# Performance work log

Hardware: AMD Instinct MI355X
Metric: run time of the kernel (lower is better)

## Reference

```python
import jax, jax.numpy as jnp
import numpy as np

BS, C, H, W = 2, 128, 80, 160
P, G = 9, 8
GC = C // G
EPS = 1e-5


def _layernorm_c(x, g, b):
    # x: (bs, C, H, W); LayerNorm over channel dim (to_3d dim=2 -> norm over c)
    m = jnp.mean(x, axis=1, keepdims=True)
    v = jnp.mean((x - m) ** 2, axis=1, keepdims=True)
    return (x - m) / jnp.sqrt(v + EPS) * g[None, :, None, None] + b[None, :, None, None]


def _conv1x1(x, w, b):
    return jnp.einsum('bchw,oc->bohw', x, w) + b[None, :, None, None]


def _bilinear_sample(feat, pts):
    # feat (bs,C,H,W); pts (bs,N,2) normalized [0,1]; zero padding outside (DAF convention)
    bs, c, h, w = feat.shape
    x = pts[..., 0] * w - 0.5
    y = pts[..., 1] * h - 0.5
    x0 = jnp.floor(x)
    y0 = jnp.floor(y)
    dx = x - x0
    dy = y - y0
    x0i = x0.astype(jnp.int32)
    y0i = y0.astype(jnp.int32)

    def corner(xi, yi, wgt):
        valid = (xi >= 0) & (xi < w) & (yi >= 0) & (yi < h)
        xc = jnp.clip(xi, 0, w - 1)
        yc = jnp.clip(yi, 0, h - 1)
        g = jax.vmap(lambda f, yy, xx: f[:, yy, xx].T)(feat, yc, xc)  # (bs,N,C)
        return g * (wgt * valid)[..., None]

    return (corner(x0i, y0i, (1 - dx) * (1 - dy))
            + corner(x0i + 1, y0i, dx * (1 - dy))
            + corner(x0i, y0i + 1, (1 - dx) * dy)
            + corner(x0i + 1, y0i + 1, dx * dy))


def _branch(match_flat, anchor, feat_value, wmap, kp_w, kp_b):
    bs = feat_value.shape[0]
    hw = H * W
    # Sparse1DKeyPointsGenerator: learned 1D offsets along the disparity (x) direction
    off = match_flat @ kp_w.T + kp_b  # (bs, HW, P)
    anc = anchor.reshape(bs, hw, P, 2)
    kp = jnp.stack([anc[..., 0] + off, anc[..., 1]], axis=-1)  # (bs,HW,P,2)
    # group-softmax attention weights over num_pts
    wts = wmap.transpose(0, 2, 3, 1).reshape(bs, hw, P, G)  # channel c = p*G + g
    wts = jax.nn.softmax(wts, axis=2)
    # deformable aggregation: bilinear gather at key points + group-weighted sum over pts
    sampled = _bilinear_sample(feat_value, kp.reshape(bs, hw * P, 2))
    sampled = sampled.reshape(bs, hw, P, G, GC)
    out = jnp.einsum('bnpgc,bnpg->bngc', sampled, wts).reshape(bs, hw, C)
    out = out.reshape(bs, H, W, C).transpose(0, 3, 1, 2)
    return out, kp


def _forward(mask, match, context, geometric, context_anchor_points, geometric_anchor_points,
             ln_g, ln_b, lnc_g, lnc_b, lng_g, lng_b,
             wc_w, wc_b, wg_w, wg_b, vc_w, vc_b, vg_w, vg_b,
             out_w, out_b, kpc_w, kpc_b, kpg_w, kpg_b):
    bs = match.shape[0]
    hw = H * W
    match_n = _layernorm_c(match, ln_g, ln_b)
    context_n = _layernorm_c(context, lnc_g, lnc_b)
    geometric_n = _layernorm_c(geometric, lng_g, lng_b)
    ctx_val = _conv1x1(context_n, vc_w, vc_b)
    geo_val = _conv1x1(geometric_n, vg_w, vg_b)
    match_flat = match_n.reshape(bs, C, hw).transpose(0, 2, 1)  # (bs,HW,C)
    wc = _conv1x1(match_n, wc_w, wc_b)  # (bs,G*P,H,W)
    wg = _conv1x1(match_n, wg_w, wg_b)
    ctx_out, ctx_kp = _branch(match_flat, context_anchor_points, ctx_val, wc, kpc_w, kpc_b)
    geo_out, geo_kp = _branch(match_flat, geometric_anchor_points, geo_val, wg, kpg_w, kpg_b)
    out = jnp.concatenate([ctx_out * mask, geo_out], axis=1)
    out = _conv1x1(out, out_w, out_b)  # proj_drop is identity (p=0)
    return out, ctx_kp.reshape(bs, H, W, P, 2), geo_kp.reshape(bs, H, W, P, 2)


def setup_inputs() -> dict:
    key = jax.random.key(0)
    ks = jax.random.split(key, 20)

    def wn(k, shape):
        return jax.random.normal(k, shape, jnp.float32) * 0.02

    return {
        'mask': jax.random.uniform(ks[0], (BS, 1, H, W), jnp.float32),
        'match': jax.random.normal(ks[1], (BS, C, H, W), jnp.float32),
        'context': jax.random.normal(ks[2], (BS, C, H, W), jnp.float32),
        'geometric': jax.random.normal(ks[3], (BS, C, H, W), jnp.float32),
        'context_anchor_points': jax.random.uniform(ks[4], (BS, H, W, P, 2), jnp.float32),
        'geometric_anchor_points': jax.random.uniform(ks[5], (BS, H, W, P, 2), jnp.float32),
        'ln_g': jnp.ones((C,), jnp.float32), 'ln_b': jnp.zeros((C,), jnp.float32),
        'lnc_g': jnp.ones((C,), jnp.float32), 'lnc_b': jnp.zeros((C,), jnp.float32),
        'lng_g': jnp.ones((C,), jnp.float32), 'lng_b': jnp.zeros((C,), jnp.float32),
        'wc_w': wn(ks[6], (G * P, C)), 'wc_b': jnp.zeros((G * P,), jnp.float32),
        'wg_w': wn(ks[7], (G * P, C)), 'wg_b': jnp.zeros((G * P,), jnp.float32),
        'vc_w': wn(ks[8], (C, C)), 'vc_b': jnp.zeros((C,), jnp.float32),
        'vg_w': wn(ks[9], (C, C)), 'vg_b': jnp.zeros((C,), jnp.float32),
        'out_w': wn(ks[10], (C, 2 * C)), 'out_b': jnp.zeros((C,), jnp.float32),
        'kpc_w': wn(ks[11], (P, C)), 'kpc_b': jnp.zeros((P,), jnp.float32),
        'kpg_w': wn(ks[12], (P, C)), 'kpg_b': jnp.zeros((P,), jnp.float32),
    }


def reference(mask, match, context, geometric, context_anchor_points, geometric_anchor_points,
              ln_g, ln_b, lnc_g, lnc_b, lng_g, lng_b,
              wc_w, wc_b, wg_w, wg_b, vc_w, vc_b, vg_w, vg_b,
              out_w, out_b, kpc_w, kpc_b, kpg_w, kpg_b):
    return _forward(mask, match, context, geometric, context_anchor_points, geometric_anchor_points,
                    ln_g, ln_b, lnc_g, lnc_b, lng_g, lng_b,
                    wc_w, wc_b, wg_w, wg_b, vc_w, vc_b, vg_w, vg_b,
                    out_w, out_b, kpc_w, kpc_b, kpg_w, kpg_b)
```

## Files before the change

kernel.cpp:

```cpp
#include <hip/hip_runtime.h>
#include <hip/hip_bf16.h>

typedef __hip_bfloat16 bf16;
typedef __bf16 b16x8 __attribute__((ext_vector_type(8)));
typedef __bf16 b16x4 __attribute__((ext_vector_type(4)));
typedef float f32x4 __attribute__((ext_vector_type(4)));
typedef float f32x2 __attribute__((ext_vector_type(2)));

#define HWs   12800
#define NPIX  25600
#define IMG_H 80
#define IMG_W 160

#define OFF_VCB  0
#define OFF_VGB  16384
#define OFF_MATB 32768
#define OFF_OUTB 53504
#define NW_BF16  86272

__global__ __launch_bounds__(256) void k_prep(
    const float* __restrict__ vc_w, const float* __restrict__ vg_w,
    const float* __restrict__ wc_w, const float* __restrict__ wg_w,
    const float* __restrict__ kpc_w, const float* __restrict__ kpg_w,
    const float* __restrict__ out_w,
    const float* __restrict__ wc_b, const float* __restrict__ wg_b,
    const float* __restrict__ kpc_b, const float* __restrict__ kpg_b,
    bf16* __restrict__ wbuf, float* __restrict__ bias176)
{
    int i = blockIdx.x * 256 + threadIdx.x;
    if (i < 16384) {
        wbuf[i] = __float2bfloat16(vc_w[i]);
    } else if (i < 32768) {
        wbuf[i] = __float2bfloat16(vg_w[i - 16384]);
    } else if (i < 53504) {
        int j = i - 32768; int row = j >> 7; int c = j & 127;
        float v;
        if (row < 72)       v = wc_w[row * 128 + c];
        else if (row < 144) v = wg_w[(row - 72) * 128 + c];
        else if (row < 153) v = kpc_w[(row - 144) * 128 + c];
        else                v = kpg_w[(row - 153) * 128 + c];
        wbuf[i] = __float2bfloat16(v);
    } else if (i < NW_BF16) {
        wbuf[i] = __float2bfloat16(out_w[i - 53504]);
    } else if (i < NW_BF16 + 176) {
        int j = i - NW_BF16;
        float v = 0.f;
        if (j < 72)       v = wc_b[j];
        else if (j < 144) v = wg_b[j - 72];
        else if (j < 153) v = kpc_b[j - 144];
        else if (j < 162) v = kpg_b[j - 153];
        bias176[j] = v;
    }
}

__global__ __launch_bounds__(256) void k_stage1(
    const float* __restrict__ match, const float* __restrict__ context, const float* __restrict__ geometric,
    const float* __restrict__ ln_g, const float* __restrict__ ln_b,
    const float* __restrict__ lnc_g, const float* __restrict__ lnc_b,
    const float* __restrict__ lng_g, const float* __restrict__ lng_b,
    const float* __restrict__ vc_b, const float* __restrict__ vg_b,
    const bf16* __restrict__ wbuf, const float* __restrict__ bias176,
    const float* __restrict__ anc_c, const float* __restrict__ anc_g,
    unsigned char* __restrict__ ctx8, unsigned char* __restrict__ geo8,
    bf16* __restrict__ wts_g, float* __restrict__ coords_g,
    float* __restrict__ kp_out)
{
    __shared__ __align__(16) bf16 tile_s[32 * 136];
    __shared__ __align__(16) bf16 logit_s[32 * 148];
    __shared__ float offs_s[32 * 18];
    __shared__ float red1[8][32];
    __shared__ float red2[8][32];

    int bx = blockIdx.x;
    int seg = bx % 3;
    int tile = bx / 3;
    int t = threadIdx.x;
    int pixbase = tile * 32;

    const float* X  = (seg == 0) ? context : (seg == 1) ? geometric : match;
    const float* gg = (seg == 0) ? lnc_g   : (seg == 1) ? lng_g     : ln_g;
    const float* bb = (seg == 0) ? lnc_b   : (seg == 1) ? lng_b     : ln_b;

    int p = t & 31;
    int cq = t >> 5;
    int b = pixbase >= HWs;
    int hw = pixbase - b * HWs;
    const float* base = X + ((size_t)b * 128) * HWs + hw + p;
    float xv[16];
#pragma unroll
    for (int j = 0; j < 16; j++) xv[j] = base[(size_t)(cq * 16 + j) * HWs];

    int wv = t >> 6;
    int lane = t & 63;
    int s = wv >> 1;
    int h = wv & 1;
    int lrow = lane & 15;
    int lq = lane >> 4;
    const bf16* Wb = (seg == 0) ? wbuf + OFF_VCB
                   : (seg == 1) ? wbuf + OFF_VGB
                                : wbuf + OFF_MATB;
    b16x8 wf[4][4];
#pragma unroll
    for (int i = 0; i < 4; i++) {
        int o = (h + 2 * i) * 16 + lrow;
        const bf16* wr = Wb + (size_t)o * 128;
#pragma unroll
        for (int kk = 0; kk < 4; kk++)
            wf[i][kk] = *(const b16x8*)(wr + (kk * 4 + lq) * 8);
    }

    {
        float s1 = 0.f, s2 = 0.f;
#pragma unroll
        for (int j = 0; j < 16; j++) { s1 += xv[j]; s2 += xv[j] * xv[j]; }
        red1[cq][p] = s1; red2[cq][p] = s2;
        __syncthreads();
        float S1 = 0.f, S2 = 0.f;
#pragma unroll
        for (int q = 0; q < 8; q++) { S1 += red1[q][p]; S2 += red2[q][p]; }
        float mean = S1 * (1.f / 128.f);
        float var  = fmaxf(S2 * (1.f / 128.f) - mean * mean, 0.f);
        float rstd = rsqrtf(var + 1e-5f);
#pragma unroll
        for (int j = 0; j < 16; j++) {
            int c = cq * 16 + j;
            float y = (xv[j] - mean) * rstd * gg[c] + bb[c];
            tile_s[p * 136 + c] = __float2bfloat16(y);
        }
        __syncthreads();
    }

    const b16x8* arow = (const b16x8*)(tile_s + (s * 16 + lrow) * 136);
    b16x8 af[4];
#pragma unroll
    for (int kk = 0; kk < 4; kk++) af[kk] = arow[kk * 4 + lq];

    int prow = s * 16 + lrow;

    if (seg < 2) {
        unsigned char* val = (seg == 0) ? ctx8 : geo8;
        const float* vb = (seg == 0) ? vc_b : vg_b;
        size_t prix = (size_t)(pixbase + prow) * 128;
#pragma unroll
        for (int i = 0; i < 4; i++) {
            int obase = (h + 2 * i) * 16 + lq * 4;
            f32x4 acc = {0.f, 0.f, 0.f, 0.f};
#pragma unroll
            for (int kk = 0; kk < 4; kk++)
                acc = __builtin_amdgcn_mfma_f32_16x16x32_bf16(wf[i][kk], af[kk], acc, 0, 0, 0);
            f32x4 bv = *(const f32x4*)(vb + obase);
            int u = __builtin_amdgcn_cvt_pk_fp8_f32(acc[0] + bv[0], acc[1] + bv[1], 0, false);
            u = __builtin_amdgcn_cvt_pk_fp8_f32(acc[2] + bv[2], acc[3] + bv[3], u, true);
            *(unsigned int*)(val + prix + obase) = (unsigned int)u;
        }
        return;
    }

#pragma unroll
    for (int i = 0; i < 4; i++) {
        int obase = (h + 2 * i) * 16 + lq * 4;
        f32x4 acc = {0.f, 0.f, 0.f, 0.f};
#pragma unroll
        for (int kk = 0; kk < 4; kk++)
            acc = __builtin_amdgcn_mfma_f32_16x16x32_bf16(wf[i][kk], af[kk], acc, 0, 0, 0);
        f32x4 bv = *(const f32x4*)(bias176 + obase);
        b16x4 pk4;
#pragma unroll
        for (int r = 0; r < 4; r++) pk4[r] = (__bf16)(acc[r] + bv[r]);
        *(b16x4*)(logit_s + prow * 148 + obase) = pk4;
    }
    for (int ot = h + 8; ot < 11; ot += 2) {
        int obase = ot * 16 + lq * 4;
        const bf16* wr = Wb + (size_t)(ot * 16 + lrow) * 128;
        f32x4 acc = {0.f, 0.f, 0.f, 0.f};
#pragma unroll
        for (int kk = 0; kk < 4; kk++)
            acc = __builtin_amdgcn_mfma_f32_16x16x32_bf16(*(const b16x8*)(wr + (kk * 4 + lq) * 8), af[kk], acc, 0, 0, 0);
        f32x4 bv = *(const f32x4*)(bias176 + obase);
        if (ot == 8) {
            b16x4 pk4;
#pragma unroll
            for (int r = 0; r < 4; r++) pk4[r] = (__bf16)(acc[r] + bv[r]);
            *(b16x4*)(logit_s + prow * 148 + obase) = pk4;
        } else if (ot == 9) {
#pragma unroll
            for (int r = 0; r < 4; r++)
                offs_s[prow * 18 + (obase - 144) + r] = acc[r] + bv[r];
        } else {
            if (lq == 0) {
                offs_s[prow * 18 + 16] = acc[0] + bv[0];
                offs_s[prow * 18 + 17] = acc[1] + bv[1];
            }
        }
    }
    __syncthreads();

#pragma unroll
    for (int i = 0; i < 2; i++) {
        int task = t + 256 * i;
        int lp = task >> 4;
        int sub = task & 15;
        int br = sub >> 3;
        int g = sub & 7;
        const bf16* basel = logit_s + lp * 148 + br * 72 + g;
        float v[9];
        float m = -1e30f;
#pragma unroll
        for (int pp = 0; pp < 9; pp++) { v[pp] = __bfloat162float(basel[pp * 8]); m = fmaxf(m, v[pp]); }
        float ssum = 0.f;
#pragma unroll
        for (int pp = 0; pp < 9; pp++) { v[pp] = __expf(v[pp] - m); ssum += v[pp]; }
        float inv = 1.f / ssum;
        int pix = pixbase + lp;
        bf16* wbp = wts_g + ((size_t)pix * 2 + br) * 72 + g * 9;
#pragma unroll
        for (int pp = 0; pp < 9; pp++) wbp[pp] = __float2bfloat16(v[pp] * inv);
    }

    for (int i = 0; i < 3; i++) {
        int task = t + 256 * i;
        if (task < 576) {
            int lp = task / 18;
            int sub2 = task - lp * 18;
            int br = sub2 / 9;
            int pp = sub2 - br * 9;
            int pix = pixbase + lp;
            float off = offs_s[lp * 18 + br * 9 + pp];
            const float* anc = br ? anc_g : anc_c;
            f32x2 a2 = *(const f32x2*)(anc + (size_t)pix * 18 + pp * 2);
            float kx = a2[0] + off;
            f32x2 kp2 = {kx, a2[1]};
            *(f32x2*)(kp_out + (size_t)br * (NPIX * 18) + (size_t)pix * 18 + pp * 2) = kp2;
            f32x2 c2 = {kx * 160.f - 0.5f, a2[1] * 80.f - 0.5f};
            *(f32x2*)(coords_g + ((size_t)pix * 2 + br) * 18 + pp * 2) = c2;
        }
    }
}

__global__ __launch_bounds__(256) void k_fuse(
    const unsigned char* __restrict__ ctx8, const unsigned char* __restrict__ geo8,
    const bf16* __restrict__ wts_g, const float* __restrict__ coords_g,
    const float* __restrict__ mask,
    const bf16* __restrict__ outb, const float* __restrict__ out_b,
    float* __restrict__ out)
{
    __shared__ __align__(16) bf16 agg_s[16 * 264];

    int t = threadIdx.x;
    int wv = t >> 6;
    int lane = t & 63;
    int q = lane >> 4;
    int sub = lane & 15;
    int c0 = sub * 8;
    int g = sub >> 1;

    int pixbase = blockIdx.x * 16;
    int qw = wv * 4 + q;
    int pix = pixbase + qw;
    int b = pixbase >= HWs;
    int rowbase = b * HWs;

#pragma unroll
    for (int br = 0; br < 2; br++) {
        const unsigned char* val = br ? geo8 : ctx8;
        int tk = pix * 2 + br;
        const float* cb = coords_g + (size_t)tk * 18;
        const bf16* wb = wts_g + (size_t)tk * 72 + g * 9;

        float wtv[9];
#pragma unroll
        for (int pp = 0; pp < 9; pp++) wtv[pp] = __bfloat162float(wb[pp]);

        float acc[8] = {0.f, 0.f, 0.f, 0.f, 0.f, 0.f, 0.f, 0.f};
        for (int pp = 0; pp < 9; pp++) {
            f32x2 cc = *(const f32x2*)(cb + pp * 2);
            float fx = floorf(cc[0]), fy = floorf(cc[1]);
            float dx = cc[0] - fx, dy = cc[1] - fy;
            int x0 = (int)fx, y0 = (int)fy;
            float wt = wtv[pp];
#pragma unroll
            for (int c4 = 0; c4 < 4; c4++) {
                int xi = x0 + (c4 & 1);
                int yi = y0 + (c4 >> 1);
                bool ok = (xi >= 0) & (xi < IMG_W) & (yi >= 0) & (yi < IMG_H);
                int xc = min(max(xi, 0), IMG_W - 1);
                int yc = min(max(yi, 0), IMG_H - 1);
                float wx = (c4 & 1) ? dx : 1.f - dx;
                float wy = (c4 >> 1) ? dy : 1.f - dy;
                float wgt = ok ? wx * wy * wt : 0.f;
                uint2 u = *(const uint2*)(val + (size_t)(rowbase + yc * IMG_W + xc) * 128 + c0);
                f32x2 v01 = __builtin_amdgcn_cvt_pk_f32_fp8(u.x, false);
                f32x2 v23 = __builtin_amdgcn_cvt_pk_f32_fp8(u.x, true);
                f32x2 v45 = __builtin_amdgcn_cvt_pk_f32_fp8(u.y, false);
                f32x2 v67 = __builtin_amdgcn_cvt_pk_f32_fp8(u.y, true);
                acc[0] += wgt * v01[0]; acc[1] += wgt * v01[1];
                acc[2] += wgt * v23[0]; acc[3] += wgt * v23[1];
                acc[4] += wgt * v45[0]; acc[5] += wgt * v45[1];
                acc[6] += wgt * v67[0]; acc[7] += wgt * v67[1];
            }
        }
        float mv = (br == 0) ? mask[pix] : 1.f;
        b16x8 pk;
#pragma unroll
        for (int j = 0; j < 8; j++) pk[j] = (__bf16)(acc[j] * mv);
        *(b16x8*)(agg_s + qw * 264 + br * 128 + c0) = pk;
    }
    __syncthreads();

    int lrow = lane & 15;
    int lq = lane >> 4;
    b16x8 af[8];
#pragma unroll
    for (int kk = 0; kk < 8; kk++)
        af[kk] = *(const b16x8*)(agg_s + lrow * 264 + (kk * 4 + lq) * 8);
#pragma unroll
    for (int i = 0; i < 2; i++) {
        int o = (wv + 4 * i) * 16 + lrow;
        const bf16* wrow = outb + (size_t)o * 256;
        f32x4 acc = {0.f, 0.f, 0.f, 0.f};
#pragma unroll
        for (int kk = 0; kk < 8; kk++)
            acc = __builtin_amdgcn_mfma_f32_16x16x32_bf16(af[kk], *(const b16x8*)(wrow + (kk * 4 + lq) * 8), acc, 0, 0, 0);
        float bias = out_b[o];
        f32x4 st;
#pragma unroll
        for (int r = 0; r < 4; r++) st[r] = acc[r] + bias;
        int hw0 = pixbase + lq * 4 - rowbase;
        *(f32x4*)(out + (size_t)b * (128 * HWs) + (size_t)o * HWs + hw0) = st;
    }
}

extern "C" void kernel_launch(void* const* d_in, const int* in_sizes, int n_in,
                              void* d_out, int out_size, void* d_ws, size_t ws_size,
                              hipStream_t stream)
{
    const float* mask      = (const float*)d_in[0];
    const float* match     = (const float*)d_in[1];
    const float* context   = (const float*)d_in[2];
    const float* geometric = (const float*)d_in[3];
    const float* anc_c     = (const float*)d_in[4];
    const float* anc_g     = (const float*)d_in[5];
    const float* ln_g  = (const float*)d_in[6];
    const float* ln_b  = (const float*)d_in[7];
    const float* lnc_g = (const float*)d_in[8];
    const float* lnc_b = (const float*)d_in[9];
    const float* lng_g = (const float*)d_in[10];
    const float* lng_b = (const float*)d_in[11];
    const float* wc_w  = (const float*)d_in[12];
    const float* wc_b  = (const float*)d_in[13];
    const float* wg_w  = (const float*)d_in[14];
    const float* wg_b  = (const float*)d_in[15];
    const float* vc_w  = (const float*)d_in[16];
    const float* vc_b  = (const float*)d_in[17];
    const float* vg_w  = (const float*)d_in[18];
    const float* vg_b  = (const float*)d_in[19];
    const float* out_w = (const float*)d_in[20];
    const float* out_b = (const float*)d_in[21];
    const float* kpc_w = (const float*)d_in[22];
    const float* kpc_b = (const float*)d_in[23];
    const float* kpg_w = (const float*)d_in[24];
    const float* kpg_b = (const float*)d_in[25];

    char* w = (char*)d_ws;
    unsigned char* ctx8 = (unsigned char*)(w);
    unsigned char* geo8 = (unsigned char*)(w + 3276800);
    bf16*  wts_g    = (bf16*)(w + 6553600);
    float* coords_g = (float*)(w + 13926400);
    bf16*  wbuf     = (bf16*)(w + 30720000);
    float* bias176  = (float*)(w + 30892544);

    float* outp = (float*)d_out;
    float* kp_out = outp + (size_t)2 * 128 * HWs;

    k_prep<<<(NW_BF16 + 176 + 255) / 256, 256, 0, stream>>>(
        vc_w, vg_w, wc_w, wg_w, kpc_w, kpg_w, out_w,
        wc_b, wg_b, kpc_b, kpg_b, wbuf, bias176);
    k_stage1<<<2400, 256, 0, stream>>>(match, context, geometric,
                                       ln_g, ln_b, lnc_g, lnc_b, lng_g, lng_b,
                                       vc_b, vg_b, wbuf, bias176,
                                       anc_c, anc_g,
                                       ctx8, geo8, wts_g, coords_g, kp_out);
    k_fuse<<<1600, 256, 0, stream>>>(ctx8, geo8, wts_g, coords_g, mask,
                                     wbuf + OFF_OUTB, out_b, outp);
}
```

Baseline: 199.1 us.

## Drop weight prep kernel, coalesce stage1 stores, widen fuse gathers

Removes the separate weight-conversion kernel and converts fp32 weights to bf16 on the fly inside both kernels. The fp8 value tiles and softmax weights are staged through swizzled shared memory so the global stores are coalesced 16-byte writes, and LN reduction buffers alias the logit buffer. The coordinates buffer is removed, so k_fuse recomputes sample coordinates from kp_out. k_fuse is also reorganised so each thread handles one branch and 16 channels with 16-byte gathers instead of looping over both branches with 8-byte loads. In exchange, weights are reloaded as fp32 and converted repeatedly in every block, and there are extra barriers.

Result: slower. 228.6 us (+14.8%).

```diff
diff --git a/kernel.cpp b/kernel.cpp
--- a/kernel.cpp
+++ b/kernel.cpp
@@ -3,7 +3,6 @@
 
 typedef __hip_bfloat16 bf16;
 typedef __bf16 b16x8 __attribute__((ext_vector_type(8)));
-typedef __bf16 b16x4 __attribute__((ext_vector_type(4)));
 typedef float f32x4 __attribute__((ext_vector_type(4)));
 typedef float f32x2 __attribute__((ext_vector_type(2)));
 
@@ -12,45 +11,25 @@
 #define IMG_H 80
 #define IMG_W 160
 
-#define OFF_VCB  0
-#define OFF_VGB  16384
-#define OFF_MATB 32768
-#define OFF_OUTB 53504
-#define NW_BF16  86272
-
-__global__ __launch_bounds__(256) void k_prep(
-    const float* __restrict__ vc_w, const float* __restrict__ vg_w,
-    const float* __restrict__ wc_w, const float* __restrict__ wg_w,
-    const float* __restrict__ kpc_w, const float* __restrict__ kpg_w,
-    const float* __restrict__ out_w,
-    const float* __restrict__ wc_b, const float* __restrict__ wg_b,
-    const float* __restrict__ kpc_b, const float* __restrict__ kpg_b,
-    bf16* __restrict__ wbuf, float* __restrict__ bias176)
+static __device__ inline b16x8 ldw8(const float* __restrict__ p)
 {
-    int i = blockIdx.x * 256 + threadIdx.x;
-    if (i < 16384) {
-        wbuf[i] = __float2bfloat16(vc_w[i]);
-    } else if (i < 32768) {
-        wbuf[i] = __float2bfloat16(vg_w[i - 16384]);
-    } else if (i < 53504) {
-        int j = i - 32768; int row = j >> 7; int c = j & 127;
-        float v;
-        if (row < 72)       v = wc_w[row * 128 + c];
-        else if (row < 144) v = wg_w[(row - 72) * 128 + c];
-        else if (row < 153) v = kpc_w[(row - 144) * 128 + c];
-        else                v = kpg_w[(row - 153) * 128 + c];
-        wbuf[i] = __float2bfloat16(v);
-    } else if (i < NW_BF16) {
-        wbuf[i] = __float2bfloat16(out_w[i - 53504]);
-    } else if (i < NW_BF16 + 176) {
-        int j = i - NW_BF16;
-        float v = 0.f;
-        if (j < 72)       v = wc_b[j];
-        else if (j < 144) v = wg_b[j - 72];
-        else if (j < 153) v = kpc_b[j - 144];
-        else if (j < 162) v = kpg_b[j - 153];
-        bias176[j] = v;
-    }
+    f32x4 a = *(const f32x4*)p;
+    f32x4 c = *(const f32x4*)(p + 4);
+    b16x8 r;
+    r[0] = (__bf16)a[0]; r[1] = (__bf16)a[1]; r[2] = (__bf16)a[2]; r[3] = (__bf16)a[3];
+    r[4] = (__bf16)c[0]; r[5] = (__bf16)c[1]; r[6] = (__bf16)c[2]; r[7] = (__bf16)c[3];
+    return r;
+}
+
+static __device__ inline const float* mat_row(
+    const float* __restrict__ wc, const float* __restrict__ wg,
+    const float* __restrict__ kpc, const float* __restrict__ kpg, int o)
+{
+    o = min(o, 161);
+    if (o < 72)  return wc  + (size_t)o * 128;
+    if (o < 144) return wg  + (size_t)(o - 72) * 128;
+    if (o < 153) return kpc + (size_t)(o - 144) * 128;
+    return kpg + (size_t)(o - 153) * 128;
 }
 
 __global__ __launch_bounds__(256) void k_stage1(
@@ -58,18 +37,25 @@
     const float* __restrict__ ln_g, const float* __restrict__ ln_b,
     const float* __restrict__ lnc_g, const float* __restrict__ lnc_b,
     const float* __restrict__ lng_g, const float* __restrict__ lng_b,
+    const float* __restrict__ vc_w, const float* __restrict__ vg_w,
     const float* __restrict__ vc_b, const float* __restrict__ vg_b,
-    const bf16* __restrict__ wbuf, const float* __restrict__ bias176,
+    const float* __restrict__ wc_w, const float* __restrict__ wg_w,
+    const float* __restrict__ kpc_w, const float* __restrict__ kpg_w,
+    const float* __restrict__ wc_b, const float* __restrict__ wg_b,
+    const float* __restrict__ kpc_b, const float* __restrict__ kpg_b,
     const float* __restrict__ anc_c, const float* __restrict__ anc_g,
     unsigned char* __restrict__ ctx8, unsigned char* __restrict__ geo8,
-    bf16* __restrict__ wts_g, float* __restrict__ coords_g,
-    float* __restrict__ kp_out)
+    bf16* __restrict__ wts_g, float* __restrict__ kp_out)
 {
     __shared__ __align__(16) bf16 tile_s[32 * 136];
-    __shared__ __align__(16) bf16 logit_s[32 * 148];
+    __shared__ __align__(16) char u_s[32 * 152 * 2];
     __shared__ float offs_s[32 * 18];
-    __shared__ float red1[8][32];
-    __shared__ float red2[8][32];
+    __shared__ float bias_s[176];
+
+    bf16* logit_s = (bf16*)u_s;
+    float (*red1)[32] = (float(*)[32])u_s;
+    float (*red2)[32] = (float(*)[32])(u_s + 1024);
+    unsigned char* fp8_s = (unsigned char*)u_s;
 
     int bx = blockIdx.x;
     int seg = bx % 3;
@@ -96,17 +82,26 @@
     int h = wv & 1;
     int lrow = lane & 15;
     int lq = lane >> 4;
-    const bf16* Wb = (seg == 0) ? wbuf + OFF_VCB
-                   : (seg == 1) ? wbuf + OFF_VGB
-                                : wbuf + OFF_MATB;
     b16x8 wf[4][4];
 #pragma unroll
     for (int i = 0; i < 4; i++) {
         int o = (h + 2 * i) * 16 + lrow;
-        const bf16* wr = Wb + (size_t)o * 128;
+        const float* wr = (seg == 0) ? vc_w + (size_t)o * 128
+                        : (seg == 1) ? vg_w + (size_t)o * 128
+                        : (o < 72)   ? wc_w + (size_t)o * 128
+                                     : wg_w + (size_t)(o - 72) * 128;
 #pragma unroll
         for (int kk = 0; kk < 4; kk++)
-            wf[i][kk] = *(const b16x8*)(wr + (kk * 4 + lq) * 8);
+            wf[i][kk] = ldw8(wr + (kk * 4 + lq) * 8);
+    }
+
+    if (seg == 2 && t < 176) {
+        float v = 0.f;
+        if (t < 72)       v = wc_b[t];
+        else if (t < 144) v = wg_b[t - 72];
+        else if (t < 153) v = kpc_b[t - 144];
+        else if (t < 162) v = kpg_b[t - 153];
+        bias_s[t] = v;
     }
 
     {
@@ -140,7 +135,7 @@
     if (seg < 2) {
         unsigned char* val = (seg == 0) ? ctx8 : geo8;
         const float* vb = (seg == 0) ? vc_b : vg_b;
-        size_t prix = (size_t)(pixbase + prow) * 128;
+        int swz = (prow & 7) << 4;
 #pragma unroll
         for (int i = 0; i < 4; i++) {
             int obase = (h + 2 * i) * 16 + lq * 4;
@@ -151,8 +146,13 @@
             f32x4 bv = *(const f32x4*)(vb + obase);
             int u = __builtin_amdgcn_cvt_pk_fp8_f32(acc[0] + bv[0], acc[1] + bv[1], 0, false);
             u = __builtin_amdgcn_cvt_pk_fp8_f32(acc[2] + bv[2], acc[3] + bv[3], u, true);
-            *(unsigned int*)(val + prix + obase) = (unsigned int)u;
-        }
+            *(unsigned int*)(fp8_s + prow * 128 + (obase ^ swz)) = (unsigned int)u;
+        }
+        __syncthreads();
+        int row = t >> 3;
+        int col = t & 7;
+        uint4 v4 = *(const uint4*)(fp8_s + row * 128 + ((col ^ (row & 7)) * 16));
+        *(uint4*)(val + (size_t)(pixbase + row) * 128 + col * 16) = v4;
         return;
     }
 
@@ -163,25 +163,23 @@
 #pragma unroll
         for (int kk = 0; kk < 4; kk++)
             acc = __builtin_amdgcn_mfma_f32_16x16x32_bf16(wf[i][kk], af[kk], acc, 0, 0, 0);
-        f32x4 bv = *(const f32x4*)(bias176 + obase);
-        b16x4 pk4;
-#pragma unroll
-        for (int r = 0; r < 4; r++) pk4[r] = (__bf16)(acc[r] + bv[r]);
-        *(b16x4*)(logit_s + prow * 148 + obase) = pk4;
+        f32x4 bv = *(const f32x4*)(bias_s + obase);
+#pragma unroll
+        for (int r = 0; r < 4; r++)
+            logit_s[prow * 152 + obase + r] = __float2bfloat16(acc[r] + bv[r]);
     }
     for (int ot = h + 8; ot < 11; ot += 2) {
         int obase = ot * 16 + lq * 4;
-        const bf16* wr = Wb + (size_t)(ot * 16 + lrow) * 128;
+        const float* wr = mat_row(wc_w, wg_w, kpc_w, kpg_w, ot * 16 + lrow);
         f32x4 acc = {0.f, 0.f, 0.f, 0.f};
 #pragma unroll
         for (int kk = 0; kk < 4; kk++)
-            acc = __builtin_amdgcn_mfma_f32_16x16x32_bf16(*(const b16x8*)(wr + (kk * 4 + lq) * 8), af[kk], acc, 0, 0, 0);
-        f32x4 bv = *(const f32x4*)(bias176 + obase);
+            acc = __builtin_amdgcn_mfma_f32_16x16x32_bf16(ldw8(wr + (kk * 4 + lq) * 8), af[kk], acc, 0, 0, 0);
+        f32x4 bv = *(const f32x4*)(bias_s + obase);
         if (ot == 8) {
-            b16x4 pk4;
-#pragma unroll
-            for (int r = 0; r < 4; r++) pk4[r] = (__bf16)(acc[r] + bv[r]);
-            *(b16x4*)(logit_s + prow * 148 + obase) = pk4;
+#pragma unroll
+            for (int r = 0; r < 4; r++)
+                logit_s[prow * 152 + obase + r] = __float2bfloat16(acc[r] + bv[r]);
         } else if (ot == 9) {
 #pragma unroll
             for (int r = 0; r < 4; r++)
@@ -195,6 +193,7 @@
     }
     __syncthreads();
 
+    float sm[2][9];
 #pragma unroll
     for (int i = 0; i < 2; i++) {
         int task = t + 256 * i;
@@ -202,7 +201,7 @@
         int sub = task & 15;
         int br = sub >> 3;
         int g = sub & 7;
-        const bf16* basel = logit_s + lp * 148 + br * 72 + g;
+        const bf16* basel = logit_s + lp * 152 + br * 72 + g;
         float v[9];
         float m = -1e30f;
 #pragma unroll
@@ -211,10 +210,31 @@
 #pragma unroll
         for (int pp = 0; pp < 9; pp++) { v[pp] = __expf(v[pp] - m); ssum += v[pp]; }
         float inv = 1.f / ssum;
-        int pix = pixbase + lp;
-        bf16* wbp = wts_g + ((size_t)pix * 2 + br) * 72 + g * 9;
-#pragma unroll
-        for (int pp = 0; pp < 9; pp++) wbp[pp] = __float2bfloat16(v[pp] * inv);
+#pragma unroll
+        for (int pp = 0; pp < 9; pp++) sm[i][pp] = v[pp] * inv;
+    }
+    __syncthreads();
+#pragma unroll
+    for (int i = 0; i < 2; i++) {
+        int task = t + 256 * i;
+        int lp = task >> 4;
+        int sub = task & 15;
+        int br = sub >> 3;
+        int g = sub & 7;
+        bf16* dst = logit_s + lp * 152 + br * 72 + g * 9;
+#pragma unroll
+        for (int pp = 0; pp < 9; pp++) dst[pp] = __float2bfloat16(sm[i][pp]);
+    }
+    __syncthreads();
+#pragma unroll
+    for (int i = 0; i < 3; i++) {
+        int idx = t + 256 * i;
+        if (idx < 576) {
+            int lp = idx / 18;
+            int c8 = idx - lp * 18;
+            *(b16x8*)(wts_g + (size_t)pixbase * 144 + (size_t)idx * 8) =
+                *(const b16x8*)(logit_s + lp * 152 + c8 * 8);
+        }
     }
 
     for (int i = 0; i < 3; i++) {
@@ -228,20 +248,17 @@
             float off = offs_s[lp * 18 + br * 9 + pp];
             const float* anc = br ? anc_g : anc_c;
             f32x2 a2 = *(const f32x2*)(anc + (size_t)pix * 18 + pp * 2);
-            float kx = a2[0] + off;
-            f32x2 kp2 = {kx, a2[1]};
+            f32x2 kp2 = {a2[0] + off, a2[1]};
             *(f32x2*)(kp_out + (size_t)br * (NPIX * 18) + (size_t)pix * 18 + pp * 2) = kp2;
-            f32x2 c2 = {kx * 160.f - 0.5f, a2[1] * 80.f - 0.5f};
-            *(f32x2*)(coords_g + ((size_t)pix * 2 + br) * 18 + pp * 2) = c2;
         }
     }
 }
 
 __global__ __launch_bounds__(256) void k_fuse(
     const unsigned char* __restrict__ ctx8, const unsigned char* __restrict__ geo8,
-    const bf16* __restrict__ wts_g, const float* __restrict__ coords_g,
+    const bf16* __restrict__ wts_g, const float* __restrict__ kp_out,
     const float* __restrict__ mask,
-    const bf16* __restrict__ outb, const float* __restrict__ out_b,
+    const float* __restrict__ out_w, const float* __restrict__ out_b,
     float* __restrict__ out)
 {
     __shared__ __align__(16) bf16 agg_s[16 * 264];
@@ -249,62 +266,70 @@
     int t = threadIdx.x;
     int wv = t >> 6;
     int lane = t & 63;
-    int q = lane >> 4;
-    int sub = lane & 15;
-    int c0 = sub * 8;
-    int g = sub >> 1;
+    int task = wv * 8 + (lane >> 3);
+    int br = task >> 4;
+    int pixidx = task & 15;
+    int g = lane & 7;
+    int c0 = g * 16;
 
     int pixbase = blockIdx.x * 16;
-    int qw = wv * 4 + q;
-    int pix = pixbase + qw;
+    int pix = pixbase + pixidx;
     int b = pixbase >= HWs;
     int rowbase = b * HWs;
 
-#pragma unroll
-    for (int br = 0; br < 2; br++) {
-        const unsigned char* val = br ? geo8 : ctx8;
-        int tk = pix * 2 + br;
-        const float* cb = coords_g + (size_t)tk * 18;
-        const bf16* wb = wts_g + (size_t)tk * 72 + g * 9;
-
-        float wtv[9];
-#pragma unroll
-        for (int pp = 0; pp < 9; pp++) wtv[pp] = __bfloat162float(wb[pp]);
-
-        float acc[8] = {0.f, 0.f, 0.f, 0.f, 0.f, 0.f, 0.f, 0.f};
-        for (int pp = 0; pp < 9; pp++) {
-            f32x2 cc = *(const f32x2*)(cb + pp * 2);
-            float fx = floorf(cc[0]), fy = floorf(cc[1]);
-            float dx = cc[0] - fx, dy = cc[1] - fy;
-            int x0 = (int)fx, y0 = (int)fy;
-            float wt = wtv[pp];
-#pragma unroll
-            for (int c4 = 0; c4 < 4; c4++) {
-                int xi = x0 + (c4 & 1);
-                int yi = y0 + (c4 >> 1);
-                bool ok = (xi >= 0) & (xi < IMG_W) & (yi >= 0) & (yi < IMG_H);
-                int xc = min(max(xi, 0), IMG_W - 1);
-                int yc = min(max(yi, 0), IMG_H - 1);
-                float wx = (c4 & 1) ? dx : 1.f - dx;
-                float wy = (c4 >> 1) ? dy : 1.f - dy;
-                float wgt = ok ? wx * wy * wt : 0.f;
-                uint2 u = *(const uint2*)(val + (size_t)(rowbase + yc * IMG_W + xc) * 128 + c0);
-                f32x2 v01 = __builtin_amdgcn_cvt_pk_f32_fp8(u.x, false);
-                f32x2 v23 = __builtin_amdgcn_cvt_pk_f32_fp8(u.x, true);
-                f32x2 v45 = __builtin_amdgcn_cvt_pk_f32_fp8(u.y, false);
-                f32x2 v67 = __builtin_amdgcn_cvt_pk_f32_fp8(u.y, true);
-                acc[0] += wgt * v01[0]; acc[1] += wgt * v01[1];
-                acc[2] += wgt * v23[0]; acc[3] += wgt * v23[1];
-                acc[4] += wgt * v45[0]; acc[5] += wgt * v45[1];
-                acc[6] += wgt * v67[0]; acc[7] += wgt * v67[1];
+    const unsigned char* val = br ? geo8 : ctx8;
+    const bf16* wb = wts_g + (size_t)(pix * 2 + br) * 72 + g * 9;
+    const float* cb = kp_out + (size_t)br * (NPIX * 18) + (size_t)pix * 18;
+
+    float wtv[9];
+#pragma unroll
+    for (int pp = 0; pp < 9; pp++) wtv[pp] = __bfloat162float(wb[pp]);
+
+    float acc[16];
+#pragma unroll
+    for (int j = 0; j < 16; j++) acc[j] = 0.f;
+
+#pragma unroll
+    for (int pp = 0; pp < 9; pp++) {
+        f32x2 kp2 = *(const f32x2*)(cb + pp * 2);
+        float px = kp2[0] * 160.f - 0.5f;
+        float py = kp2[1] * 80.f - 0.5f;
+        float fx = floorf(px), fy = floorf(py);
+        float dx = px - fx, dy = py - fy;
+        int x0 = (int)fx, y0 = (int)fy;
+        float wt = wtv[pp];
+#pragma unroll
+        for (int c4 = 0; c4 < 4; c4++) {
+            int xi = x0 + (c4 & 1);
+            int yi = y0 + (c4 >> 1);
+            bool ok = (xi >= 0) & (xi < IMG_W) & (yi >= 0) & (yi < IMG_H);
+            int xc = min(max(xi, 0), IMG_W - 1);
+            int yc = min(max(yi, 0), IMG_H - 1);
+            float wx = (c4 & 1) ? dx : 1.f - dx;
+            float wy = (c4 >> 1) ? dy : 1.f - dy;
+            float wgt = ok ? wx * wy * wt : 0.f;
+            uint4 u = *(const uint4*)(val + (size_t)(rowbase + yc * IMG_W + xc) * 128 + c0);
+            unsigned int uw[4] = {u.x, u.y, u.z, u.w};
+#pragma unroll
+            for (int w2 = 0; w2 < 4; w2++) {
+                f32x2 lo = __builtin_amdgcn_cvt_pk_f32_fp8(uw[w2], false);
+                f32x2 hi = __builtin_amdgcn_cvt_pk_f32_fp8(uw[w2], true);
+                acc[w2 * 4 + 0] += wgt * lo[0];
+                acc[w2 * 4 + 1] += wgt * lo[1];
+                acc[w2 * 4 + 2] += wgt * hi[0];
+                acc[w2 * 4 + 3] += wgt * hi[1];
             }
         }
-        float mv = (br == 0) ? mask[pix] : 1.f;
-        b16x8 pk;
-#pragma unroll
-        for (int j = 0; j < 8; j++) pk[j] = (__bf16)(acc[j] * mv);
-        *(b16x8*)(agg_s + qw * 264 + br * 128 + c0) = pk;
-    }
+    }
+    float mv = br ? 1.f : mask[pix];
+    b16x8 pk0, pk1;
+#pragma unroll
+    for (int j = 0; j < 8; j++) {
+        pk0[j] = (__bf16)(acc[j] * mv);
+        pk1[j] = (__bf16)(acc[8 + j] * mv);
+    }
+    *(b16x8*)(agg_s + pixidx * 264 + br * 128 + c0) = pk0;
+    *(b16x8*)(agg_s + pixidx * 264 + br * 128 + c0 + 8) = pk1;
     __syncthreads();
 
     int lrow = lane & 15;
@@ -316,15 +341,15 @@
 #pragma unroll
     for (int i = 0; i < 2; i++) {
         int o = (wv + 4 * i) * 16 + lrow;
-        const bf16* wrow = outb + (size_t)o * 256;
-        f32x4 acc = {0.f, 0.f, 0.f, 0.f};
+        const float* wrow = out_w + (size_t)o * 256;
+        f32x4 acc4 = {0.f, 0.f, 0.f, 0.f};
 #pragma unroll
         for (int kk = 0; kk < 8; kk++)
-            acc = __builtin_amdgcn_mfma_f32_16x16x32_bf16(af[kk], *(const b16x8*)(wrow + (kk * 4 + lq) * 8), acc, 0, 0, 0);
+            acc4 = __builtin_amdgcn_mfma_f32_16x16x32_bf16(af[kk], ldw8(wrow + (kk * 4 + lq) * 8), acc4, 0, 0, 0);
         float bias = out_b[o];
         f32x4 st;
 #pragma unroll
-        for (int r = 0; r < 4; r++) st[r] = acc[r] + bias;
+        for (int r = 0; r < 4; r++) st[r] = acc4[r] + bias;
         int hw0 = pixbase + lq * 4 - rowbase;
         *(f32x4*)(out + (size_t)b * (128 * HWs) + (size_t)o * HWs + hw0) = st;
     }
@@ -365,21 +390,17 @@
     unsigned char* ctx8 = (unsigned char*)(w);
     unsigned char* geo8 = (unsigned char*)(w + 3276800);
     bf16*  wts_g    = (bf16*)(w + 6553600);
-    float* coords_g = (float*)(w + 13926400);
-    bf16*  wbuf     = (bf16*)(w + 30720000);
-    float* bias176  = (float*)(w + 30892544);
 
     float* outp = (float*)d_out;
     float* kp_out = outp + (size_t)2 * 128 * HWs;
 
-    k_prep<<<(NW_BF16 + 176 + 255) / 256, 256, 0, stream>>>(
-        vc_w, vg_w, wc_w, wg_w, kpc_w, kpg_w, out_w,
-        wc_b, wg_b, kpc_b, kpg_b, wbuf, bias176);
     k_stage1<<<2400, 256, 0, stream>>>(match, context, geometric,
                                        ln_g, ln_b, lnc_g, lnc_b, lng_g, lng_b,
-                                       vc_b, vg_b, wbuf, bias176,
+                                       vc_w, vg_w, vc_b, vg_b,
+                                       wc_w, wg_w, kpc_w, kpg_w,
+                                       wc_b, wg_b, kpc_b, kpg_b,
                                        anc_c, anc_g,
-                                       ctx8, geo8, wts_g, coords_g, kp_out);
-    k_fuse<<<1600, 256, 0, stream>>>(ctx8, geo8, wts_g, coords_g, mask,
-                                     wbuf + OFF_OUTB, out_b, outp);
+                                       ctx8, geo8, wts_g, kp_out);
+    k_fuse<<<1600, 256, 0, stream>>>(ctx8, geo8, wts_g, kp_out, mask,
+                                     out_w, out_b, outp);
 }
```

## Stage fp8 value writes through swizzled LDS and drop coords buffer

Applied to the files above, without the earlier changes.

The fp8 value projections in k_stage1 are first written into a swizzled shared-memory tile and then stored to global memory as coalesced 16-byte rows, replacing scattered 4-byte stores. The separate coords_g buffer is removed. k_fuse now reads the keypoint output directly and recomputes pixel coordinates, which cuts one global write and read stream. It also adds a minimum-blocks hint of 7 to k_stage1's launch bounds, which may constrain register allocation, and adds a barrier in the value-projection path.

Result: slower. 236.2 us (+18.7%).

```diff
diff --git a/kernel.cpp b/kernel.cpp
--- a/kernel.cpp
+++ b/kernel.cpp
@@ -53,7 +53,7 @@
     }
 }
 
-__global__ __launch_bounds__(256) void k_stage1(
+__global__ __launch_bounds__(256, 7) void k_stage1(
     const float* __restrict__ match, const float* __restrict__ context, const float* __restrict__ geometric,
     const float* __restrict__ ln_g, const float* __restrict__ ln_b,
     const float* __restrict__ lnc_g, const float* __restrict__ lnc_b,
@@ -62,14 +62,15 @@
     const bf16* __restrict__ wbuf, const float* __restrict__ bias176,
     const float* __restrict__ anc_c, const float* __restrict__ anc_g,
     unsigned char* __restrict__ ctx8, unsigned char* __restrict__ geo8,
-    bf16* __restrict__ wts_g, float* __restrict__ coords_g,
-    float* __restrict__ kp_out)
+    bf16* __restrict__ wts_g, float* __restrict__ kp_out)
 {
     __shared__ __align__(16) bf16 tile_s[32 * 136];
     __shared__ __align__(16) bf16 logit_s[32 * 148];
     __shared__ float offs_s[32 * 18];
     __shared__ float red1[8][32];
     __shared__ float red2[8][32];
+
+    unsigned char* fp8_s = (unsigned char*)logit_s;
 
     int bx = blockIdx.x;
     int seg = bx % 3;
@@ -140,7 +141,7 @@
     if (seg < 2) {
         unsigned char* val = (seg == 0) ? ctx8 : geo8;
         const float* vb = (seg == 0) ? vc_b : vg_b;
-        size_t prix = (size_t)(pixbase + prow) * 128;
+        int swz = (prow & 7) << 4;
 #pragma unroll
         for (int i = 0; i < 4; i++) {
             int obase = (h + 2 * i) * 16 + lq * 4;
@@ -151,8 +152,13 @@
             f32x4 bv = *(const f32x4*)(vb + obase);
             int u = __builtin_amdgcn_cvt_pk_fp8_f32(acc[0] + bv[0], acc[1] + bv[1], 0, false);
             u = __builtin_amdgcn_cvt_pk_fp8_f32(acc[2] + bv[2], acc[3] + bv[3], u, true);
-            *(unsigned int*)(val + prix + obase) = (unsigned int)u;
-        }
+            *(unsigned int*)(fp8_s + prow * 128 + (obase ^ swz)) = (unsigned int)u;
+        }
+        __syncthreads();
+        int row = t >> 3;
+        int col = t & 7;
+        uint4 v4 = *(const uint4*)(fp8_s + row * 128 + ((col ^ (row & 7)) * 16));
+        *(uint4*)(val + (size_t)(pixbase + row) * 128 + col * 16) = v4;
         return;
     }
 
@@ -228,18 +234,15 @@
             float off = offs_s[lp * 18 + br * 9 + pp];
             const float* anc = br ? anc_g : anc_c;
             f32x2 a2 = *(const f32x2*)(anc + (size_t)pix * 18 + pp * 2);
-            float kx = a2[0] + off;
-            f32x2 kp2 = {kx, a2[1]};
+            f32x2 kp2 = {a2[0] + off, a2[1]};
             *(f32x2*)(kp_out + (size_t)br * (NPIX * 18) + (size_t)pix * 18 + pp * 2) = kp2;
-            f32x2 c2 = {kx * 160.f - 0.5f, a2[1] * 80.f - 0.5f};
-            *(f32x2*)(coords_g + ((size_t)pix * 2 + br) * 18 + pp * 2) = c2;
         }
     }
 }
 
 __global__ __launch_bounds__(256) void k_fuse(
     const unsigned char* __restrict__ ctx8, const unsigned char* __restrict__ geo8,
-    const bf16* __restrict__ wts_g, const float* __restrict__ coords_g,
+    const bf16* __restrict__ wts_g, const float* __restrict__ kp_out,
     const float* __restrict__ mask,
     const bf16* __restrict__ outb, const float* __restrict__ out_b,
     float* __restrict__ out)
@@ -263,9 +266,8 @@
 #pragma unroll
     for (int br = 0; br < 2; br++) {
         const unsigned char* val = br ? geo8 : ctx8;
-        int tk = pix * 2 + br;
-        const float* cb = coords_g + (size_t)tk * 18;
-        const bf16* wb = wts_g + (size_t)tk * 72 + g * 9;
+        const bf16* wb = wts_g + (size_t)(pix * 2 + br) * 72 + g * 9;
+        const float* cb = kp_out + (size_t)br * (NPIX * 18) + (size_t)pix * 18;
 
         float wtv[9];
 #pragma unroll
@@ -273,9 +275,11 @@
 
         float acc[8] = {0.f, 0.f, 0.f, 0.f, 0.f, 0.f, 0.f, 0.f};
         for (int pp = 0; pp < 9; pp++) {
-            f32x2 cc = *(const f32x2*)(cb + pp * 2);
-            float fx = floorf(cc[0]), fy = floorf(cc[1]);
-            float dx = cc[0] - fx, dy = cc[1] - fy;
+            f32x2 kp2 = *(const f32x2*)(cb + pp * 2);
+            float px = kp2[0] * 160.f - 0.5f;
+            float py = kp2[1] * 80.f - 0.5f;
+            float fx = floorf(px), fy = floorf(py);
+            float dx = px - fx, dy = py - fy;
             int x0 = (int)fx, y0 = (int)fy;
             float wt = wtv[pp];
 #pragma unroll
@@ -317,14 +321,14 @@
     for (int i = 0; i < 2; i++) {
         int o = (wv + 4 * i) * 16 + lrow;
         const bf16* wrow = outb + (size_t)o * 256;
-        f32x4 acc = {0.f, 0.f, 0.f, 0.f};
+        f32x4 acc4 = {0.f, 0.f, 0.f, 0.f};
 #pragma unroll
         for (int kk = 0; kk < 8; kk++)
-            acc = __builtin_amdgcn_mfma_f32_16x16x32_bf16(af[kk], *(const b16x8*)(wrow + (kk * 4 + lq) * 8), acc, 0, 0, 0);
+            acc4 = __builtin_amdgcn_mfma_f32_16x16x32_bf16(af[kk], *(const b16x8*)(wrow + (kk * 4 + lq) * 8), acc4, 0, 0, 0);
         float bias = out_b[o];
         f32x4 st;
 #pragma unroll
-        for (int r = 0; r < 4; r++) st[r] = acc[r] + bias;
+        for (int r = 0; r < 4; r++) st[r] = acc4[r] + bias;
         int hw0 = pixbase + lq * 4 - rowbase;
         *(f32x4*)(out + (size_t)b * (128 * HWs) + (size_t)o * HWs + hw0) = st;
     }
@@ -365,9 +369,8 @@
     unsigned char* ctx8 = (unsigned char*)(w);
     unsigned char* geo8 = (unsigned char*)(w + 3276800);
     bf16*  wts_g    = (bf16*)(w + 6553600);
-    float* coords_g = (float*)(w + 13926400);
-    bf16*  wbuf     = (bf16*)(w + 30720000);
-    float* bias176  = (float*)(w + 30892544);
+    bf16*  wbuf     = (bf16*)(w + 13926400);
+    float* bias176  = (float*)(w + 14098944);
 
     float* outp = (float*)d_out;
     float* kp_out = outp + (size_t)2 * 128 * HWs;
@@ -379,7 +382,7 @@
                                        ln_g, ln_b, lnc_g, lnc_b, lng_g, lng_b,
                                        vc_b, vg_b, wbuf, bias176,
                                        anc_c, anc_g,
-                                       ctx8, geo8, wts_g, coords_g, kp_out);
-    k_fuse<<<1600, 256, 0, stream>>>(ctx8, geo8, wts_g, coords_g, mask,
+                                       ctx8, geo8, wts_g, kp_out);
+    k_fuse<<<1600, 256, 0, stream>>>(ctx8, geo8, wts_g, kp_out, mask,
                                      wbuf + OFF_OUTB, out_b, outp);
 }
```
